# Optimization experiments

Hardware: AMD Instinct MI355X
Metric: run time of the kernel (lower is better)

## Reference

```python
import jax, jax.numpy as jnp
import numpy as np

TEMPERATURE = 0.05
EPS = 1e-12  # F.normalize eps


def _l2norm(x):
    n = jnp.sqrt(jnp.sum(x * x, axis=-1, keepdims=True))
    return x / jnp.maximum(n, EPS)


def setup_inputs() -> dict:
    key = jax.random.key(0)
    k1, k2, k3 = jax.random.split(key, 3)
    B, S, D = 8, 1536, 1024
    h1 = jax.random.normal(k1, (B, S, D), dtype=jnp.float32)
    h2 = jax.random.normal(k2, (B, S, D), dtype=jnp.float32)
    mask = jax.random.randint(k3, (B, S), 0, 2).astype(bool)
    return {"last_hidden_states_1": h1, "last_hidden_states_2": h2, "token_mask_batch": mask}


def reference(last_hidden_states_1, last_hidden_states_2, token_mask_batch):
    # Vectorized equivalent of the per-sample python loop: padded (masked) tokens
    # simply contribute nothing to pos/neg sums or the mean.
    B, S, D = last_hidden_states_1.shape
    f1 = _l2norm(last_hidden_states_1)  # [B,S,D]
    f2 = _l2norm(last_hidden_states_2)
    feats = jnp.concatenate([f1, f2], axis=1)  # [B,2S,D]

    # positive pairs: token i in view1 vs token i in view2
    pos_sim = jnp.sum(f1 * f2, axis=-1).astype(jnp.float32) / TEMPERATURE  # [B,S]
    pos = jnp.exp(jnp.concatenate([pos_sim, pos_sim], axis=1))  # [B,2S]

    # all-pairs similarities among the 2n effective tokens
    sim = jnp.einsum("bid,bjd->bij", feats, feats).astype(jnp.float32) / TEMPERATURE  # [B,2S,2S]

    m2 = jnp.concatenate([token_mask_batch, token_mask_batch], axis=1)  # [B,2S]
    tok = jnp.arange(2 * S) % S
    same_token = tok[:, None] == tok[None, :]  # excludes self and its positive counterpart
    neg_mask = m2[:, :, None] & m2[:, None, :] & (~same_token)  # [B,2S,2S]

    Ng = jnp.sum(jnp.exp(sim) * neg_mask, axis=-1)  # [B,2S]
    per_tok = -jnp.log(pos / (Ng + pos))  # [B,2S]

    m2f = m2.astype(jnp.float32)
    per_sample = jnp.sum(per_tok * m2f, axis=1) / jnp.sum(m2f, axis=1)  # mean over 2n tokens
    return jnp.mean(per_sample)
```

## Files before the change

### kernel.cpp

```cpp
#include <hip/hip_runtime.h>
#include <hip/hip_bf16.h>
#include <math.h>

#define BATCH 8
#define SEQ   1536
#define DIM   1024
#define SEQ2  (2*SEQ)
#define TEMP_INV 20.0f
#define EXP_SCALE (TEMP_INV / 64.0f)

#define BM 128
#define BN 128
#define BK 128
#define KITERS (DIM/BK)
#define TILES  (SEQ2 / BM)
#define NPAIRS (TILES * (TILES+1) / 2)

typedef int   i32x4 __attribute__((ext_vector_type(4)));
typedef int   i32x8 __attribute__((ext_vector_type(8)));
typedef float f32x4 __attribute__((ext_vector_type(4)));

#define GLOBAL_AS __attribute__((address_space(1)))
#define LDS_AS    __attribute__((address_space(3)))

__device__ inline void async_ld16(const void* g, void* lds_uniform) {
    __builtin_amdgcn_global_load_lds((const GLOBAL_AS void*)g, (LDS_AS void*)lds_uniform, 16, 0, 0);
}

__device__ inline float wave_red64(float v) {
    #pragma unroll
    for (int m = 32; m > 0; m >>= 1) v += __shfl_xor(v, m, 64);
    return v;
}

__global__ __launch_bounds__(256) void normalize_kernel(
        const float* __restrict__ h1, const float* __restrict__ h2,
        unsigned char* __restrict__ feats, float* __restrict__ pos_cos,
        float* __restrict__ Ng, float* __restrict__ out) {
    int w = threadIdx.x >> 6, lane = threadIdx.x & 63;
    int tok = blockIdx.x * 4 + w;
    int b = tok / SEQ, s = tok - b * SEQ;

    const float4* a4 = (const float4*)(h1 + (size_t)tok * DIM);
    const float4* b4 = (const float4*)(h2 + (size_t)tok * DIM);
    float4 av[4], bv[4];
    #pragma unroll
    for (int it = 0; it < 4; it++) { av[it] = a4[lane + 64*it]; bv[it] = b4[lane + 64*it]; }

    float ss1 = 0.f, ss2 = 0.f, sd = 0.f;
    #pragma unroll
    for (int it = 0; it < 4; it++) {
        ss1 += av[it].x*av[it].x + av[it].y*av[it].y + av[it].z*av[it].z + av[it].w*av[it].w;
        ss2 += bv[it].x*bv[it].x + bv[it].y*bv[it].y + bv[it].z*bv[it].z + bv[it].w*bv[it].w;
        sd  += av[it].x*bv[it].x + av[it].y*bv[it].y + av[it].z*bv[it].z + av[it].w*bv[it].w;
    }
    ss1 = wave_red64(ss1); ss2 = wave_red64(ss2); sd = wave_red64(sd);

    float sc1 = 1.0f / fmaxf(sqrtf(ss1), 1e-12f);
    float sc2 = 1.0f / fmaxf(sqrtf(ss2), 1e-12f);
    float s18 = sc1 * 8.0f, s28 = sc2 * 8.0f;

    unsigned int* f1row = (unsigned int*)(feats + ((size_t)b * SEQ2 + s) * DIM);
    unsigned int* f2row = (unsigned int*)(feats + ((size_t)b * SEQ2 + SEQ + s) * DIM);
    #pragma unroll
    for (int it = 0; it < 4; it++) {
        int p1 = __builtin_amdgcn_cvt_pk_fp8_f32(av[it].x * s18, av[it].y * s18, 0, 0);
        p1     = __builtin_amdgcn_cvt_pk_fp8_f32(av[it].z * s18, av[it].w * s18, p1, 1);
        int p2 = __builtin_amdgcn_cvt_pk_fp8_f32(bv[it].x * s28, bv[it].y * s28, 0, 0);
        p2     = __builtin_amdgcn_cvt_pk_fp8_f32(bv[it].z * s28, bv[it].w * s28, p2, 1);
        f1row[lane + 64*it] = (unsigned int)p1;
        f2row[lane + 64*it] = (unsigned int)p2;
    }
    if (lane == 0) {
        pos_cos[tok] = sd * sc1 * sc2;
        Ng[2*tok] = 0.0f;
        Ng[2*tok + 1] = 0.0f;
        if (tok == 0) out[0] = 0.0f;
    }
}

__global__ __launch_bounds__(256, 3) void gemm_ng_kernel(
        const unsigned char* __restrict__ feats, const int* __restrict__ mask,
        float* __restrict__ Ng) {
    int bid = blockIdx.x;
    int b = bid & 7;
    int p = bid >> 3;
    int ti = 0;
    while (p >= TILES - ti) { p -= TILES - ti; ti++; }
    int tj = ti + p;
    int ibase = ti * BM, jbase = tj * BN;
    bool isdiag = (ti == tj);

    const unsigned char* fb = feats + (size_t)b * SEQ2 * DIM;

    __shared__ __align__(16) unsigned char As[BM][BK];
    __shared__ __align__(16) unsigned char Bs[BN][BK];
    __shared__ float mrow_s[BM];
    __shared__ float mcol_s[BN];

    int t = threadIdx.x;
    int lane = t & 63, w = t >> 6;
    int wrow = w >> 1, wcol = w & 1;
    int colq = lane & 15, quad = lane >> 4;

    int sr = t >> 3;
    int sc = (t & 7) ^ (sr & 7);
    const unsigned char* a0 = fb + (size_t)(ibase + sr) * DIM + sc * 16;
    const unsigned char* b0 = fb + (size_t)(jbase + sr) * DIM + sc * 16;

    auto stage = [&](int it) {
        size_t kb = (size_t)it * BK;
        #pragma unroll
        for (int q = 0; q < 4; q++) {
            async_ld16(a0 + (size_t)q * 32 * DIM + kb, (char*)&As[0][0] + q * 4096 + w * 1024);
            async_ld16(b0 + (size_t)q * 32 * DIM + kb, (char*)&Bs[0][0] + q * 4096 + w * 1024);
        }
    };

    stage(0);

    if (t < BM) {
        int i = ibase + t; int im = (i < SEQ) ? i : i - SEQ;
        mrow_s[t] = mask[b * SEQ + im] ? 1.0f : 0.0f;
    } else {
        int j = jbase + (t - BM); int jm = (j < SEQ) ? j : j - SEQ;
        mcol_s[t - BM] = mask[b * SEQ + jm] ? 1.0f : 0.0f;
    }
    __syncthreads();

    f32x4 acc[4][4] = {};
    int s0 = ((2 * quad)     ^ (colq & 7)) * 16;
    int s1 = ((2 * quad + 1) ^ (colq & 7)) * 16;

    #pragma unroll 1
    for (int it = 0; it < KITERS; it++) {
        i32x8 af[4], bg[4];
        #pragma unroll
        for (int mi = 0; mi < 4; mi++) {
            int row = wrow * 64 + mi * 16 + colq;
            i32x4 lo = *(const i32x4*)&As[row][s0];
            i32x4 hi = *(const i32x4*)&As[row][s1];
            af[mi] = __builtin_shufflevector(lo, hi, 0, 1, 2, 3, 4, 5, 6, 7);
        }
        #pragma unroll
        for (int nj = 0; nj < 4; nj++) {
            int row = wcol * 64 + nj * 16 + colq;
            i32x4 lo = *(const i32x4*)&Bs[row][s0];
            i32x4 hi = *(const i32x4*)&Bs[row][s1];
            bg[nj] = __builtin_shufflevector(lo, hi, 0, 1, 2, 3, 4, 5, 6, 7);
        }

        __syncthreads();

        if (it + 1 < KITERS) {
            stage(it + 1);
            __builtin_amdgcn_sched_barrier(0);
        }

        #pragma unroll
        for (int mi = 0; mi < 4; mi++)
            #pragma unroll
            for (int nj = 0; nj < 4; nj++)
                acc[mi][nj] = __builtin_amdgcn_mfma_scale_f32_16x16x128_f8f6f4(
                    af[mi], bg[nj], acc[mi][nj],
                    0, 0,
                    0, 0x7F7F7F7F,
                    0, 0x7F7F7F7F);

        if (it + 1 < KITERS)
            __syncthreads();
    }

    float mj[4]; int jglob[4];
    #pragma unroll
    for (int nj = 0; nj < 4; nj++) {
        int jl = wcol * 64 + nj * 16 + colq;
        mj[nj] = mcol_s[jl];
        jglob[nj] = jbase + jl;
    }
    float colsum[4] = {0.f, 0.f, 0.f, 0.f};

    #pragma unroll
    for (int mi = 0; mi < 4; mi++) {
        int il0 = wrow * 64 + mi * 16 + quad * 4;
        float rsum[4] = {0.f, 0.f, 0.f, 0.f};
        float mr[4];
        #pragma unroll
        for (int r = 0; r < 4; r++) mr[r] = mrow_s[il0 + r];
        #pragma unroll
        for (int nj = 0; nj < 4; nj++) {
            #pragma unroll
            for (int r = 0; r < 4; r++) {
                int d = (ibase + il0 + r) - jglob[nj];
                bool same = (d == 0) | (d == SEQ) | (d == -SEQ);
                float e = same ? 0.0f : __expf(acc[mi][nj][r] * EXP_SCALE);
                rsum[r] += e * mj[nj];
                colsum[nj] += e * mr[r];
            }
        }
        #pragma unroll
        for (int r = 0; r < 4; r++) {
            float v = rsum[r];
            #pragma unroll
            for (int m = 1; m < 16; m <<= 1) v += __shfl_xor(v, m, 64);
            if (colq == 0)
                atomicAdd(&Ng[b * SEQ2 + ibase + il0 + r], v);
        }
    }

    if (!isdiag) {
        #pragma unroll
        for (int nj = 0; nj < 4; nj++) {
            float v = colsum[nj];
            v += __shfl_xor(v, 16, 64);
            v += __shfl_xor(v, 32, 64);
            if (quad == 0)
                atomicAdd(&Ng[b * SEQ2 + jglob[nj]], v);
        }
    }
}

__global__ __launch_bounds__(1024) void loss_kernel(
        const float* __restrict__ Ng, const float* __restrict__ pos_cos,
        const int* __restrict__ mask, float* __restrict__ out) {
    int b = blockIdx.x, t = threadIdx.x;
    float sum = 0.f, cnt = 0.f;
    for (int i = t; i < SEQ2; i += 1024) {
        int im = (i < SEQ) ? i : i - SEQ;
        if (mask[b * SEQ + im]) {
            float ps = pos_cos[b * SEQ + im] * TEMP_INV;
            float ng = Ng[b * SEQ2 + i];
            sum += log1pf(ng * __expf(-ps));
            cnt += 1.0f;
        }
    }
    sum = wave_red64(sum); cnt = wave_red64(cnt);
    __shared__ float rs[16], rc[16];
    int lane = t & 63, w = t >> 6;
    if (lane == 0) { rs[w] = sum; rc[w] = cnt; }
    __syncthreads();
    if (t == 0) {
        float s = 0.f, c = 0.f;
        #pragma unroll
        for (int k = 0; k < 16; k++) { s += rs[k]; c += rc[k]; }
        atomicAdd(out, s / c * (1.0f / BATCH));
    }
}

extern "C" void kernel_launch(void* const* d_in, const int* in_sizes, int n_in,
                              void* d_out, int out_size, void* d_ws, size_t ws_size,
                              hipStream_t stream) {
    const float* h1  = (const float*)d_in[0];
    const float* h2  = (const float*)d_in[1];
    const int* mask  = (const int*)d_in[2];
    float* out       = (float*)d_out;

    char* ws = (char*)d_ws;
    size_t feats_bytes = (size_t)BATCH * SEQ2 * DIM;
    unsigned char* feats = (unsigned char*)ws;
    float* pos_cos    = (float*)(ws + feats_bytes);
    float* Ng         = (float*)(ws + feats_bytes + (size_t)BATCH * SEQ * 4);

    normalize_kernel<<<BATCH * SEQ / 4, 256, 0, stream>>>(h1, h2, feats, pos_cos, Ng, out);

    gemm_ng_kernel<<<NPAIRS * BATCH, 256, 0, stream>>>(feats, mask, Ng);

    loss_kernel<<<BATCH, 1024, 0, stream>>>(Ng, pos_cos, mask, out);
}
```

Measured before the change: 193.6 us.

## Shrink GEMM tiles to 64x64 single-wave blocks and drop block barriers

The GEMM+exp kernel now uses 64x64 tiles computed by a single 64-thread wavefront instead of 128x128 tiles across four waves. Block-level __syncthreads are replaced with explicit s_waitcnt on LDS and vector-memory counters, which is valid because only one wave touches the shared buffers. This removes barrier overhead and raises the block count (more upper-triangle tile pairs) for load balance, at the cost of halving operand reuse per loaded byte and roughly doubling global/LDS traffic per FLOP.

```diff
diff --git a/kernel.cpp b/kernel.cpp
--- a/kernel.cpp
+++ b/kernel.cpp
@@ -9,8 +9,8 @@
 #define TEMP_INV 20.0f
 #define EXP_SCALE (TEMP_INV / 64.0f)
 
-#define BM 128
-#define BN 128
+#define BM 64
+#define BN 64
 #define BK 128
 #define KITERS (DIM/BK)
 #define TILES  (SEQ2 / BM)
@@ -79,7 +79,7 @@
     }
 }
 
-__global__ __launch_bounds__(256, 3) void gemm_ng_kernel(
+__global__ __launch_bounds__(64, 2) void gemm_ng_kernel(
         const unsigned char* __restrict__ feats, const int* __restrict__ mask,
         float* __restrict__ Ng) {
     int bid = blockIdx.x;
@@ -98,35 +98,32 @@
     __shared__ float mrow_s[BM];
     __shared__ float mcol_s[BN];
 
-    int t = threadIdx.x;
-    int lane = t & 63, w = t >> 6;
-    int wrow = w >> 1, wcol = w & 1;
+    int lane = threadIdx.x & 63;
     int colq = lane & 15, quad = lane >> 4;
 
-    int sr = t >> 3;
-    int sc = (t & 7) ^ (sr & 7);
+    int sr = lane >> 3;
+    int sc = (lane & 7) ^ sr;
     const unsigned char* a0 = fb + (size_t)(ibase + sr) * DIM + sc * 16;
     const unsigned char* b0 = fb + (size_t)(jbase + sr) * DIM + sc * 16;
 
     auto stage = [&](int it) {
         size_t kb = (size_t)it * BK;
         #pragma unroll
-        for (int q = 0; q < 4; q++) {
-            async_ld16(a0 + (size_t)q * 32 * DIM + kb, (char*)&As[0][0] + q * 4096 + w * 1024);
-            async_ld16(b0 + (size_t)q * 32 * DIM + kb, (char*)&Bs[0][0] + q * 4096 + w * 1024);
+        for (int q = 0; q < 8; q++) {
+            async_ld16(a0 + (size_t)q * 8 * DIM + kb, (char*)&As[0][0] + q * 1024);
+            async_ld16(b0 + (size_t)q * 8 * DIM + kb, (char*)&Bs[0][0] + q * 1024);
         }
     };
 
     stage(0);
 
-    if (t < BM) {
-        int i = ibase + t; int im = (i < SEQ) ? i : i - SEQ;
-        mrow_s[t] = mask[b * SEQ + im] ? 1.0f : 0.0f;
-    } else {
-        int j = jbase + (t - BM); int jm = (j < SEQ) ? j : j - SEQ;
-        mcol_s[t - BM] = mask[b * SEQ + jm] ? 1.0f : 0.0f;
-    }
-    __syncthreads();
+    {
+        int i = ibase + lane; int im = (i < SEQ) ? i : i - SEQ;
+        mrow_s[lane] = mask[b * SEQ + im] ? 1.0f : 0.0f;
+        int j = jbase + lane; int jm = (j < SEQ) ? j : j - SEQ;
+        mcol_s[lane] = mask[b * SEQ + jm] ? 1.0f : 0.0f;
+    }
+    asm volatile("s_waitcnt vmcnt(0)" ::: "memory");
 
     f32x4 acc[4][4] = {};
     int s0 = ((2 * quad)     ^ (colq & 7)) * 16;
@@ -137,22 +134,22 @@
         i32x8 af[4], bg[4];
         #pragma unroll
         for (int mi = 0; mi < 4; mi++) {
-            int row = wrow * 64 + mi * 16 + colq;
+            int row = mi * 16 + colq;
             i32x4 lo = *(const i32x4*)&As[row][s0];
             i32x4 hi = *(const i32x4*)&As[row][s1];
             af[mi] = __builtin_shufflevector(lo, hi, 0, 1, 2, 3, 4, 5, 6, 7);
         }
         #pragma unroll
         for (int nj = 0; nj < 4; nj++) {
-            int row = wcol * 64 + nj * 16 + colq;
+            int row = nj * 16 + colq;
             i32x4 lo = *(const i32x4*)&Bs[row][s0];
             i32x4 hi = *(const i32x4*)&Bs[row][s1];
             bg[nj] = __builtin_shufflevector(lo, hi, 0, 1, 2, 3, 4, 5, 6, 7);
         }
 
-        __syncthreads();
-
         if (it + 1 < KITERS) {
+            asm volatile("s_waitcnt lgkmcnt(0)" ::: "memory");
+            __builtin_amdgcn_sched_barrier(0);
             stage(it + 1);
             __builtin_amdgcn_sched_barrier(0);
         }
@@ -168,13 +165,13 @@
                     0, 0x7F7F7F7F);
 
         if (it + 1 < KITERS)
-            __syncthreads();
+            asm volatile("s_waitcnt vmcnt(0)" ::: "memory");
     }
 
     float mj[4]; int jglob[4];
     #pragma unroll
     for (int nj = 0; nj < 4; nj++) {
-        int jl = wcol * 64 + nj * 16 + colq;
+        int jl = nj * 16 + colq;
         mj[nj] = mcol_s[jl];
         jglob[nj] = jbase + jl;
     }
@@ -182,7 +179,7 @@
 
     #pragma unroll
     for (int mi = 0; mi < 4; mi++) {
-        int il0 = wrow * 64 + mi * 16 + quad * 4;
+        int il0 = mi * 16 + quad * 4;
         float rsum[4] = {0.f, 0.f, 0.f, 0.f};
         float mr[4];
         #pragma unroll
@@ -263,7 +260,7 @@
 
     normalize_kernel<<<BATCH * SEQ / 4, 256, 0, stream>>>(h1, h2, feats, pos_cos, Ng, out);
 
-    gemm_ng_kernel<<<NPAIRS * BATCH, 256, 0, stream>>>(feats, mask, Ng);
+    gemm_ng_kernel<<<NPAIRS * BATCH, 64, 0, stream>>>(feats, mask, Ng);
 
     loss_kernel<<<BATCH, 1024, 0, stream>>>(Ng, pos_cos, mask, out);
 }
```

Result: slower. 212.9 us (+10.0%).
